# Kernel optimization log

Hardware: AMD Instinct MI355X
Metric: run time of the kernel (lower is better)

Reference implementation:

```python
import jax, jax.numpy as jnp
import numpy as np

KH = KW = 3
K = KH * KW
OG = 1  # offset_groups
WG = 1  # weight_groups
DIL = 1

def _conv_same(x, w):
    # stride-1 SAME NCHW conv, matching the keras offset/mask convs
    return jax.lax.conv_general_dilated(
        x, w, window_strides=(1, 1), padding='SAME',
        dimension_numbers=('NCHW', 'OIHW', 'NCHW'))

def _deform_conv2d(x, w, offset, mask):
    # x: [B,C,H,W]; w: [F, C//WG, KH, KW]
    # offset: [B, OG*2*K, H, W] laid out as (og, k, {dy,dx});
    # mask:   [B, OG*K, H, W]
    B, C, H, W = x.shape
    F = w.shape[0]
    pad_h = ((KH - 1) * DIL) // 2
    pad_w = ((KW - 1) * DIL) // 2
    ky = jnp.arange(KH) * DIL - pad_h
    kx = jnp.arange(KW) * DIL - pad_w
    kyy, kxx = jnp.meshgrid(ky, kx, indexing='ij')
    kyy = kyy.reshape(K).astype(x.dtype)
    kxx = kxx.reshape(K).astype(x.dtype)

    off = offset.reshape(B, OG, K, 2, H, W)
    dy = off[:, :, :, 0]  # [B,OG,K,H,W]
    dx = off[:, :, :, 1]
    oy = jnp.arange(H, dtype=x.dtype)
    ox = jnp.arange(W, dtype=x.dtype)
    y = oy[None, None, None, :, None] + kyy[None, None, :, None, None] + dy
    xq = ox[None, None, None, None, :] + kxx[None, None, :, None, None] + dx

    y0 = jnp.floor(y)
    x0 = jnp.floor(xq)
    wy = y - y0   # [B,OG,K,H,W]
    wx = xq - x0
    y0i = y0.astype(jnp.int32)
    x0i = x0.astype(jnp.int32)

    Cg = C // OG
    xg = x.reshape(B, OG, Cg, H * W)

    def gather(yi, xi):
        valid = (yi >= 0) & (yi < H) & (xi >= 0) & (xi < W)
        idx = jnp.clip(yi, 0, H - 1) * W + jnp.clip(xi, 0, W - 1)
        flat = idx.reshape(B, OG, 1, K * H * W)
        v = jnp.take_along_axis(xg, flat, axis=3)   # [B,OG,Cg,K*H*W]
        v = v.reshape(B, OG, Cg, K, H, W)
        return v * valid[:, :, None].astype(x.dtype)

    v00 = gather(y0i, x0i)
    v01 = gather(y0i, x0i + 1)
    v10 = gather(y0i + 1, x0i)
    v11 = gather(y0i + 1, x0i + 1)
    wy_ = wy[:, :, None]
    wx_ = wx[:, :, None]
    samp = (v00 * (1 - wy_) * (1 - wx_) + v01 * (1 - wy_) * wx_
            + v10 * wy_ * (1 - wx_) + v11 * wy_ * wx_)  # [B,OG,Cg,K,H,W]
    m = mask.reshape(B, OG, K, H, W)[:, :, None]
    samp = samp * m
    wr = w.reshape(F, OG, Cg, K)
    return jnp.einsum('bgckhw,fgck->bfhw', samp, wr)


def setup_inputs() -> dict:
    key = jax.random.key(0)
    k1, k2, k3, k4 = jax.random.split(key, 4)
    B, C, H, W = 8, 256, 64, 64
    F = 256
    x = jax.random.normal(k1, (B, C, H, W), dtype=jnp.float32)
    w_offset = jax.random.normal(k2, (OG * 2 * K, C, KH, KW), dtype=jnp.float32) * 0.01
    w_mask = jax.random.normal(k3, (OG * K, C, KH, KW), dtype=jnp.float32) * 0.01
    w_deform = jax.random.normal(k4, (F, C // WG, KH, KW), dtype=jnp.float32) * 0.05
    return {'x': x, 'w_offset': w_offset, 'w_mask': w_mask, 'w_deform': w_deform}


def reference(x, w_offset, w_mask, w_deform):
    offset = _conv_same(x, w_offset)                 # [B, 2K, H, W]
    mask = jax.nn.sigmoid(_conv_same(x, w_mask))     # [B, K, H, W]
    return _deform_conv2d(x, w_deform, offset, mask)
```

## Files before the change

### kernel.cpp

```cpp
#include <hip/hip_runtime.h>
#include <hip/hip_bf16.h>
#include <hip/hip_fp16.h>
#include <math.h>

constexpr int Bn = 8, Cn = 256, Hn = 64, Wn = 64, Fn = 256, Kn = 9;
constexpr int HWn = Hn * Wn;
constexpr int NM = Bn * Kn * HWn;
constexpr int NCH = 4;

using frag_ab = __attribute__((ext_vector_type(8))) short;
using frag_h  = __attribute__((ext_vector_type(8))) _Float16;
using f32x4   = __attribute__((ext_vector_type(4))) float;

__device__ inline ushort f2bf(float f) {
    union { float f; uint32_t u; } un{f};
    return (ushort)((un.u + 0x7FFF + ((un.u >> 16) & 1)) >> 16);
}
__device__ inline ushort f2h(float f) {
    __half h = __float2half_rn(f);
    return *reinterpret_cast<ushort*>(&h);
}

__global__ __launch_bounds__(256) void wpack27(const float* __restrict__ wo,
                                               const float* __restrict__ wm,
                                               ushort* __restrict__ wA) {
    int i = blockIdx.x * 256 + threadIdx.x;
    if (i >= 73728) return;
    int ci = i & 7, l = (i >> 3) & 63, mt = (i >> 9) & 1, cblk = (i >> 10) & 7, tap = i >> 13;
    int m = mt * 16 + (l & 15);
    int c = cblk * 32 + ((l >> 4) & 3) * 8 + ci;
    float v = 0.f;
    if (m < 18)      v = wo[(m * Cn + c) * 9 + tap];
    else if (m < 27) v = wm[((m - 18) * Cn + c) * 9 + tap];
    wA[i] = f2bf(v);
}

__global__ __launch_bounds__(256) void offconv27(const float* __restrict__ x,
                                                 const ushort* __restrict__ wA,
                                                 float* __restrict__ part) {
    __shared__ ushort xs[4][66][40];
    const int t = threadIdx.x;
    const int l = t & 63, w = t >> 6;
    const int li = l & 15, lg = l >> 4;
    const int rb = blockIdx.x, ch = blockIdx.y, b = blockIdx.z;
    const int h0 = rb * 2;
    const int rw = w >> 1, pt0 = (w & 1) * 2;

    f32x4 acc[2][2];
#pragma unroll
    for (int mt = 0; mt < 2; ++mt)
#pragma unroll
        for (int q = 0; q < 2; ++q) acc[mt][q] = (f32x4)0.f;

    const float* xb = x + (size_t)b * Cn * HWn;

#pragma unroll 1
    for (int cc = 0; cc < 2; ++cc) {
        const int cbase = ch * 64 + cc * 32;
        __syncthreads();
        for (int j = t; j < 1056; j += 256) {
            int cq = j / 264;
            int rem = j - cq * 264;
            int r = rem / 66, col = rem - r * 66;
            int rg = h0 - 1 + r, cg = col - 1;
            ushort u[8];
            if ((unsigned)rg < (unsigned)Hn && (unsigned)cg < (unsigned)Wn) {
                const float* xp = xb + (size_t)(cbase + cq * 8) * HWn + (rg << 6) + cg;
#pragma unroll
                for (int jj = 0; jj < 8; ++jj) u[jj] = f2bf(xp[(size_t)jj * HWn]);
            } else {
#pragma unroll
                for (int jj = 0; jj < 8; ++jj) u[jj] = 0;
            }
            *(int4*)&xs[r][col][cq * 8] =
                make_int4(u[0] | (u[1] << 16), u[2] | (u[3] << 16),
                          u[4] | (u[5] << 16), u[6] | (u[7] << 16));
        }
        __syncthreads();
        const int cblk = ch * 2 + cc;
#pragma unroll
        for (int tap = 0; tap < 9; ++tap) {
            const int ky = tap / 3, kx = tap - 3 * (tap / 3);
            frag_ab a0 = *(const frag_ab*)(wA + (size_t)((tap * 8 + cblk) * 2) * 512 + l * 8);
            frag_ab a1 = *(const frag_ab*)(wA + (size_t)((tap * 8 + cblk) * 2 + 1) * 512 + l * 8);
#pragma unroll
            for (int q = 0; q < 2; ++q) {
                frag_ab bf = *(const frag_ab*)&xs[rw + ky][(pt0 + q) * 16 + li + kx][lg * 8];
                acc[0][q] = __builtin_amdgcn_mfma_f32_16x16x32_bf16(a0, bf, acc[0][q], 0, 0, 0);
                acc[1][q] = __builtin_amdgcn_mfma_f32_16x16x32_bf16(a1, bf, acc[1][q], 0, 0, 0);
            }
        }
    }

    const int h = h0 + rw;
#pragma unroll
    for (int mt = 0; mt < 2; ++mt)
#pragma unroll
        for (int j = 0; j < 4; ++j) {
            int m = mt * 16 + lg * 4 + j;
            if (m < 27) {
#pragma unroll
                for (int q = 0; q < 2; ++q) {
                    int pixel = (pt0 + q) * 16 + li;
                    part[((size_t)((ch * Bn + b) * 27 + m) << 12) + (h << 6) + pixel] =
                        acc[mt][q][j];
                }
            }
        }
}

__global__ __launch_bounds__(256) void metafin9(const float* __restrict__ part,
                                                int4* __restrict__ mpack) {
    const int k = blockIdx.y;
    const int idx = blockIdx.x * 256 + threadIdx.x;
    const int b = idx >> 12, p = idx & 4095;
    const int h = p >> 6, w = p & 63;

    float dy = 0.f, dx = 0.f, ms = 0.f;
#pragma unroll
    for (int ch = 0; ch < NCH; ++ch) {
        size_t base = ((size_t)((ch * Bn + b) * 27) << 12) + p;
        dy += part[base + ((size_t)(2 * k) << 12)];
        dx += part[base + ((size_t)(2 * k + 1) << 12)];
        ms += part[base + ((size_t)(18 + k) << 12)];
    }
    float m = 1.f / (1.f + expf(-ms));
    float yy = (float)(h + k / 3 - 1) + dy;
    float xx = (float)(w + k % 3 - 1) + dx;
    float y0f = floorf(yy), x0f = floorf(xx);
    float wy = yy - y0f, wx = xx - x0f;
    int y0 = (int)y0f, x0 = (int)x0f;
    int y1 = y0 + 1, x1 = x0 + 1;
    bool vy0 = (unsigned)y0 < (unsigned)Hn;
    bool vx0 = (unsigned)x0 < (unsigned)Wn;
    bool vy1 = (unsigned)y1 < (unsigned)Hn;
    bool vx1 = (unsigned)x1 < (unsigned)Wn;
    int cy0 = min(max(y0, 0), Hn - 1), cx0 = min(max(x0, 0), Wn - 1);
    int cy1 = min(max(y1, 0), Hn - 1), cx1 = min(max(x1, 0), Wn - 1);
    float w00 = (vy0 && vx0) ? (1.f - wy) * (1.f - wx) * m : 0.f;
    float w01 = (vy0 && vx1) ? (1.f - wy) * wx * m : 0.f;
    float w10 = (vy1 && vx0) ? wy * (1.f - wx) * m : 0.f;
    float w11 = (vy1 && vx1) ? wy * wx * m : 0.f;
    int i00 = (cy0 << 6) + cx0, i01 = (cy0 << 6) + cx1;
    int i10 = (cy1 << 6) + cx0, i11 = (cy1 << 6) + cx1;
    union { struct { __half a, bh; } h; int i; } pz, pw;
    pz.h.a = __float2half_rn(w00); pz.h.bh = __float2half_rn(w01);
    pw.h.a = __float2half_rn(w10); pw.h.bh = __float2half_rn(w11);
    int q = ((b * 9 + k) << 12) + p;
    mpack[q] = make_int4(i00 | (i01 << 16), i10 | (i11 << 16), pz.i, pw.i);
}

__global__ __launch_bounds__(256) void packBX(const float* __restrict__ wd,
                                              const float* __restrict__ x,
                                              ushort* __restrict__ wB,
                                              __half2* __restrict__ xh) {
    const int bid = blockIdx.x, t = threadIdx.x;
    if (bid < 2304) {
        int i = bid * 256 + t;
        int ci = i & 7, fi = (i >> 3) & 15, G = (i >> 7) & 31, ft = (i >> 12) & 15, k = i >> 16;
        int f = ft * 16 + fi, c = G * 8 + ci;
        wB[i] = f2h(wd[(f * Cn + c) * 9 + k]);
    } else {
        int i = (bid - 2304) * 256 + t;
        int p = i & 4095, q = (i >> 12) & 3, b = i >> 14;
        const float* xp = x + (size_t)b * Cn * HWn + p;
        __half2* op = xh + (((size_t)b * 4096 + p) << 7) + q * 32;
#pragma unroll
        for (int j = 0; j < 32; ++j) {
            int c = q * 64 + 2 * j;
            op[j] = __float22half2_rn(make_float2(xp[(size_t)c * HWn],
                                                  xp[(size_t)(c + 1) * HWn]));
        }
    }
}

__global__ __launch_bounds__(512, 4) void dconv(const uint32_t* __restrict__ xh,
                                                const ushort* __restrict__ wB,
                                                const int4* __restrict__ mpack,
                                                float* __restrict__ out) {
    __shared__ ushort sl[2][2][64][64];
    __shared__ int4 ml[9][64];
    const int t = threadIdx.x;
    const int l = t & 63, w = t >> 6;
    const int li = l & 15, lg = l >> 4;
    const int pu = (w << 3) + (l >> 3);
    const int g  = l & 7;
    const int b = blockIdx.x;
    const int p0 = blockIdx.y << 6;

    f32x4 acc[2][4];
#pragma unroll
    for (int a = 0; a < 2; ++a)
#pragma unroll
        for (int q = 0; q < 4; ++q) acc[a][q] = (f32x4)0.f;

    const uint32_t* xb = xh + ((size_t)b << 19);

    for (int j = t; j < 576; j += 512)
        ml[j >> 6][j & 63] = mpack[((b * 9 + (j >> 6)) << 12) + p0 + (j & 63)];
    __syncthreads();

    auto STAGE = [&](int s) {
        const int k = s % 9, ch = s / 9;
        const int4 m = ml[k][pu];
        const int i00 = m.x & 0xFFFF, i01 = ((unsigned)m.x) >> 16;
        const int i10 = m.y & 0xFFFF, i11 = ((unsigned)m.y) >> 16;
        union { int i; __half2 h; } uz, uw;
        uz.i = m.z; uw.i = m.w;
        const uint32_t* base = xb + (ch << 5) + (g << 2);
        uint4 v00 = *(const uint4*)(base + (size_t)i00 * 128);
        uint4 v01 = *(const uint4*)(base + (size_t)i01 * 128);
        uint4 v10 = *(const uint4*)(base + (size_t)i10 * 128);
        uint4 v11 = *(const uint4*)(base + (size_t)i11 * 128);
        const __half2 w00 = __half2half2(__low2half(uz.h));
        const __half2 w01 = __half2half2(__high2half(uz.h));
        const __half2 w10 = __half2half2(__low2half(uw.h));
        const __half2 w11 = __half2half2(__high2half(uw.h));
        uint4 rr;
        {
            __half2 r = __hmul2(w00, *(__half2*)&v00.x);
            r = __hfma2(w01, *(__half2*)&v01.x, r);
            r = __hfma2(w10, *(__half2*)&v10.x, r);
            r = __hfma2(w11, *(__half2*)&v11.x, r);
            rr.x = *(uint32_t*)&r;
        }
        {
            __half2 r = __hmul2(w00, *(__half2*)&v00.y);
            r = __hfma2(w01, *(__half2*)&v01.y, r);
            r = __hfma2(w10, *(__half2*)&v10.y, r);
            r = __hfma2(w11, *(__half2*)&v11.y, r);
            rr.y = *(uint32_t*)&r;
        }
        {
            __half2 r = __hmul2(w00, *(__half2*)&v00.z);
            r = __hfma2(w01, *(__half2*)&v01.z, r);
            r = __hfma2(w10, *(__half2*)&v10.z, r);
            r = __hfma2(w11, *(__half2*)&v11.z, r);
            rr.z = *(uint32_t*)&r;
        }
        {
            __half2 r = __hmul2(w00, *(__half2*)&v00.w);
            r = __hfma2(w01, *(__half2*)&v01.w, r);
            r = __hfma2(w10, *(__half2*)&v10.w, r);
            r = __hfma2(w11, *(__half2*)&v11.w, r);
            rr.w = *(uint32_t*)&r;
        }
        *(uint4*)&sl[(s >> 1) & 1][s & 1][pu][(g ^ (pu & 7)) << 3] = rr;
    };

    auto COMPUTE = [&](int s) {
        const int k = s % 9, ch = s / 9;
        const ushort* wp = wB + ((size_t)((k * 16 + 2 * w) * 512 + ch * 128)) * 8;
#pragma unroll
        for (int h = 0; h < 2; ++h) {
            frag_h bq[4];
#pragma unroll
            for (int pt = 0; pt < 4; ++pt)
                bq[pt] = *(const frag_h*)&sl[(s >> 1) & 1][s & 1][pt * 16 + li]
                                           [((((h << 2) | lg) ^ (l & 7)) << 3)];
#pragma unroll
            for (int ft = 0; ft < 2; ++ft) {
                frag_h a = *(const frag_h*)(wp + (size_t)(ft * 512 + h * 64 + l) * 8);
#pragma unroll
                for (int pt = 0; pt < 4; ++pt)
                    acc[ft][pt] = __builtin_amdgcn_mfma_f32_16x16x32_f16(
                        a, bq[pt], acc[ft][pt], 0, 0, 0);
            }
        }
    };

    STAGE(0);
    STAGE(1);
    __syncthreads();
#pragma unroll 1
    for (int s = 0; s < 36; s += 2) {
        if (s + 2 < 36) {
            STAGE(s + 2);
            STAGE(s + 3);
        }
        COMPUTE(s);
        COMPUTE(s + 1);
        __syncthreads();
    }

    float* ob = out + (size_t)b * Fn * HWn + p0;
#pragma unroll
    for (int ft = 0; ft < 2; ++ft)
#pragma unroll
        for (int j = 0; j < 4; ++j) {
            int f = w * 32 + ft * 16 + lg * 4 + j;
#pragma unroll
            for (int pt = 0; pt < 4; ++pt)
                ob[(size_t)f * HWn + pt * 16 + li] = acc[ft][pt][j];
        }
}

extern "C" void kernel_launch(void* const* d_in, const int* in_sizes, int n_in,
                              void* d_out, int out_size, void* d_ws, size_t ws_size,
                              hipStream_t stream) {
    const float* x  = (const float*)d_in[0];
    const float* wo = (const float*)d_in[1];
    const float* wm = (const float*)d_in[2];
    const float* wd = (const float*)d_in[3];
    float* out = (float*)d_out;

    int4*     mpack = (int4*)d_ws;
    char*     region = (char*)d_ws + (size_t)NM * 16;
    float*    part  = (float*)region;
    ushort*   wBp   = (ushort*)region;
    __half2*  xhh   = (__half2*)(region + 1179648);
    uint32_t* xhu   = (uint32_t*)(region + 1179648);
    ushort*   wA27  = (ushort*)(region + 18874368);

    wpack27<<<dim3(288), dim3(256), 0, stream>>>(wo, wm, wA27);
    offconv27<<<dim3(32, NCH, Bn), dim3(256), 0, stream>>>(x, wA27, part);
    metafin9<<<dim3(Bn * HWn / 256, 9), dim3(256), 0, stream>>>(part, mpack);
    packBX<<<dim3(2816), dim3(256), 0, stream>>>(wd, x, wBp, xhh);
    dconv<<<dim3(Bn, HWn / 64), dim3(512), 0, stream>>>(xhu, wBp, mpack, out);
}
```

Measured before the change: 105.7 us.

## Fuse offset conv with metadata finalisation and reuse packed fp16 input

Measured after the change: 110.2 us. +4.3%, slower.

```diff
diff --git a/kernel.cpp b/kernel.cpp
--- a/kernel.cpp
+++ b/kernel.cpp
@@ -6,162 +6,39 @@
 constexpr int Bn = 8, Cn = 256, Hn = 64, Wn = 64, Fn = 256, Kn = 9;
 constexpr int HWn = Hn * Wn;
 constexpr int NM = Bn * Kn * HWn;
-constexpr int NCH = 4;
-
-using frag_ab = __attribute__((ext_vector_type(8))) short;
+
 using frag_h  = __attribute__((ext_vector_type(8))) _Float16;
 using f32x4   = __attribute__((ext_vector_type(4))) float;
 
-__device__ inline ushort f2bf(float f) {
-    union { float f; uint32_t u; } un{f};
-    return (ushort)((un.u + 0x7FFF + ((un.u >> 16) & 1)) >> 16);
-}
 __device__ inline ushort f2h(float f) {
     __half h = __float2half_rn(f);
     return *reinterpret_cast<ushort*>(&h);
 }
 
-__global__ __launch_bounds__(256) void wpack27(const float* __restrict__ wo,
+__global__ __launch_bounds__(256) void packall(const float* __restrict__ wd,
+                                               const float* __restrict__ wo,
                                                const float* __restrict__ wm,
-                                               ushort* __restrict__ wA) {
-    int i = blockIdx.x * 256 + threadIdx.x;
-    if (i >= 73728) return;
-    int ci = i & 7, l = (i >> 3) & 63, mt = (i >> 9) & 1, cblk = (i >> 10) & 7, tap = i >> 13;
-    int m = mt * 16 + (l & 15);
-    int c = cblk * 32 + ((l >> 4) & 3) * 8 + ci;
-    float v = 0.f;
-    if (m < 18)      v = wo[(m * Cn + c) * 9 + tap];
-    else if (m < 27) v = wm[((m - 18) * Cn + c) * 9 + tap];
-    wA[i] = f2bf(v);
-}
-
-__global__ __launch_bounds__(256) void offconv27(const float* __restrict__ x,
-                                                 const ushort* __restrict__ wA,
-                                                 float* __restrict__ part) {
-    __shared__ ushort xs[4][66][40];
-    const int t = threadIdx.x;
-    const int l = t & 63, w = t >> 6;
-    const int li = l & 15, lg = l >> 4;
-    const int rb = blockIdx.x, ch = blockIdx.y, b = blockIdx.z;
-    const int h0 = rb * 2;
-    const int rw = w >> 1, pt0 = (w & 1) * 2;
-
-    f32x4 acc[2][2];
-#pragma unroll
-    for (int mt = 0; mt < 2; ++mt)
-#pragma unroll
-        for (int q = 0; q < 2; ++q) acc[mt][q] = (f32x4)0.f;
-
-    const float* xb = x + (size_t)b * Cn * HWn;
-
-#pragma unroll 1
-    for (int cc = 0; cc < 2; ++cc) {
-        const int cbase = ch * 64 + cc * 32;
-        __syncthreads();
-        for (int j = t; j < 1056; j += 256) {
-            int cq = j / 264;
-            int rem = j - cq * 264;
-            int r = rem / 66, col = rem - r * 66;
-            int rg = h0 - 1 + r, cg = col - 1;
-            ushort u[8];
-            if ((unsigned)rg < (unsigned)Hn && (unsigned)cg < (unsigned)Wn) {
-                const float* xp = xb + (size_t)(cbase + cq * 8) * HWn + (rg << 6) + cg;
-#pragma unroll
-                for (int jj = 0; jj < 8; ++jj) u[jj] = f2bf(xp[(size_t)jj * HWn]);
-            } else {
-#pragma unroll
-                for (int jj = 0; jj < 8; ++jj) u[jj] = 0;
-            }
-            *(int4*)&xs[r][col][cq * 8] =
-                make_int4(u[0] | (u[1] << 16), u[2] | (u[3] << 16),
-                          u[4] | (u[5] << 16), u[6] | (u[7] << 16));
-        }
-        __syncthreads();
-        const int cblk = ch * 2 + cc;
-#pragma unroll
-        for (int tap = 0; tap < 9; ++tap) {
-            const int ky = tap / 3, kx = tap - 3 * (tap / 3);
-            frag_ab a0 = *(const frag_ab*)(wA + (size_t)((tap * 8 + cblk) * 2) * 512 + l * 8);
-            frag_ab a1 = *(const frag_ab*)(wA + (size_t)((tap * 8 + cblk) * 2 + 1) * 512 + l * 8);
-#pragma unroll
-            for (int q = 0; q < 2; ++q) {
-                frag_ab bf = *(const frag_ab*)&xs[rw + ky][(pt0 + q) * 16 + li + kx][lg * 8];
-                acc[0][q] = __builtin_amdgcn_mfma_f32_16x16x32_bf16(a0, bf, acc[0][q], 0, 0, 0);
-                acc[1][q] = __builtin_amdgcn_mfma_f32_16x16x32_bf16(a1, bf, acc[1][q], 0, 0, 0);
-            }
-        }
-    }
-
-    const int h = h0 + rw;
-#pragma unroll
-    for (int mt = 0; mt < 2; ++mt)
-#pragma unroll
-        for (int j = 0; j < 4; ++j) {
-            int m = mt * 16 + lg * 4 + j;
-            if (m < 27) {
-#pragma unroll
-                for (int q = 0; q < 2; ++q) {
-                    int pixel = (pt0 + q) * 16 + li;
-                    part[((size_t)((ch * Bn + b) * 27 + m) << 12) + (h << 6) + pixel] =
-                        acc[mt][q][j];
-                }
-            }
-        }
-}
-
-__global__ __launch_bounds__(256) void metafin9(const float* __restrict__ part,
-                                                int4* __restrict__ mpack) {
-    const int k = blockIdx.y;
-    const int idx = blockIdx.x * 256 + threadIdx.x;
-    const int b = idx >> 12, p = idx & 4095;
-    const int h = p >> 6, w = p & 63;
-
-    float dy = 0.f, dx = 0.f, ms = 0.f;
-#pragma unroll
-    for (int ch = 0; ch < NCH; ++ch) {
-        size_t base = ((size_t)((ch * Bn + b) * 27) << 12) + p;
-        dy += part[base + ((size_t)(2 * k) << 12)];
-        dx += part[base + ((size_t)(2 * k + 1) << 12)];
-        ms += part[base + ((size_t)(18 + k) << 12)];
-    }
-    float m = 1.f / (1.f + expf(-ms));
-    float yy = (float)(h + k / 3 - 1) + dy;
-    float xx = (float)(w + k % 3 - 1) + dx;
-    float y0f = floorf(yy), x0f = floorf(xx);
-    float wy = yy - y0f, wx = xx - x0f;
-    int y0 = (int)y0f, x0 = (int)x0f;
-    int y1 = y0 + 1, x1 = x0 + 1;
-    bool vy0 = (unsigned)y0 < (unsigned)Hn;
-    bool vx0 = (unsigned)x0 < (unsigned)Wn;
-    bool vy1 = (unsigned)y1 < (unsigned)Hn;
-    bool vx1 = (unsigned)x1 < (unsigned)Wn;
-    int cy0 = min(max(y0, 0), Hn - 1), cx0 = min(max(x0, 0), Wn - 1);
-    int cy1 = min(max(y1, 0), Hn - 1), cx1 = min(max(x1, 0), Wn - 1);
-    float w00 = (vy0 && vx0) ? (1.f - wy) * (1.f - wx) * m : 0.f;
-    float w01 = (vy0 && vx1) ? (1.f - wy) * wx * m : 0.f;
-    float w10 = (vy1 && vx0) ? wy * (1.f - wx) * m : 0.f;
-    float w11 = (vy1 && vx1) ? wy * wx * m : 0.f;
-    int i00 = (cy0 << 6) + cx0, i01 = (cy0 << 6) + cx1;
-    int i10 = (cy1 << 6) + cx0, i11 = (cy1 << 6) + cx1;
-    union { struct { __half a, bh; } h; int i; } pz, pw;
-    pz.h.a = __float2half_rn(w00); pz.h.bh = __float2half_rn(w01);
-    pw.h.a = __float2half_rn(w10); pw.h.bh = __float2half_rn(w11);
-    int q = ((b * 9 + k) << 12) + p;
-    mpack[q] = make_int4(i00 | (i01 << 16), i10 | (i11 << 16), pz.i, pw.i);
-}
-
-__global__ __launch_bounds__(256) void packBX(const float* __restrict__ wd,
-                                              const float* __restrict__ x,
-                                              ushort* __restrict__ wB,
-                                              __half2* __restrict__ xh) {
+                                               const float* __restrict__ x,
+                                               ushort* __restrict__ wB,
+                                               ushort* __restrict__ wA,
+                                               __half2* __restrict__ xh) {
     const int bid = blockIdx.x, t = threadIdx.x;
     if (bid < 2304) {
         int i = bid * 256 + t;
         int ci = i & 7, fi = (i >> 3) & 15, G = (i >> 7) & 31, ft = (i >> 12) & 15, k = i >> 16;
         int f = ft * 16 + fi, c = G * 8 + ci;
         wB[i] = f2h(wd[(f * Cn + c) * 9 + k]);
+    } else if (bid < 2592) {
+        int i = (bid - 2304) * 256 + t;
+        int ci = i & 7, l = (i >> 3) & 63, mt = (i >> 9) & 1, cblk = (i >> 10) & 7, tap = i >> 13;
+        int m = mt * 16 + (l & 15);
+        int c = cblk * 32 + ((l >> 4) & 3) * 8 + ci;
+        float v = 0.f;
+        if (m < 18)      v = wo[(m * Cn + c) * 9 + tap];
+        else if (m < 27) v = wm[((m - 18) * Cn + c) * 9 + tap];
+        wA[i] = f2h(v);
     } else {
-        int i = (bid - 2304) * 256 + t;
+        int i = (bid - 2592) * 256 + t;
         int p = i & 4095, q = (i >> 12) & 3, b = i >> 14;
         const float* xp = x + (size_t)b * Cn * HWn + p;
         __half2* op = xh + (((size_t)b * 4096 + p) << 7) + q * 32;
@@ -171,6 +48,99 @@
             op[j] = __float22half2_rn(make_float2(xp[(size_t)c * HWn],
                                                   xp[(size_t)(c + 1) * HWn]));
         }
+    }
+}
+
+__global__ __launch_bounds__(256) void offmeta(const uint32_t* __restrict__ xh,
+                                               const ushort* __restrict__ wA,
+                                               int4* __restrict__ mpack) {
+    __shared__ ushort xs[4][66][36];
+    __shared__ float macc[32][128];
+    const int t = threadIdx.x;
+    const int l = t & 63, w = t >> 6;
+    const int li = l & 15, lg = l >> 4;
+    const int rb = blockIdx.x, b = blockIdx.y;
+    const int h0 = rb * 2;
+    const int rw = w >> 1, pt0 = (w & 1) * 2;
+
+    f32x4 acc[2][2];
+#pragma unroll
+    for (int mt = 0; mt < 2; ++mt)
+#pragma unroll
+        for (int q = 0; q < 2; ++q) acc[mt][q] = (f32x4)0.f;
+
+    const uint32_t* xbb = xh + ((size_t)b << 19);
+
+#pragma unroll 1
+    for (int cs = 0; cs < 8; ++cs) {
+        __syncthreads();
+        for (int j = t; j < 1056; j += 256) {
+            int pj = j >> 2, qd = j & 3;
+            int r = pj / 66, col = pj - r * 66;
+            int rg = h0 - 1 + r, cg = col - 1;
+            uint4 v = make_uint4(0, 0, 0, 0);
+            if ((unsigned)rg < (unsigned)Hn && (unsigned)cg < (unsigned)Wn)
+                v = *(const uint4*)(xbb + ((size_t)((rg << 6) + cg) << 7) + cs * 16 + qd * 4);
+            *(uint4*)&xs[r][col][qd * 8] = v;
+        }
+        __syncthreads();
+#pragma unroll
+        for (int tap = 0; tap < 9; ++tap) {
+            const int ky = tap / 3, kx = tap - 3 * (tap / 3);
+            frag_h a0 = *(const frag_h*)(wA + (size_t)((tap * 8 + cs) * 2) * 512 + l * 8);
+            frag_h a1 = *(const frag_h*)(wA + (size_t)((tap * 8 + cs) * 2 + 1) * 512 + l * 8);
+#pragma unroll
+            for (int q = 0; q < 2; ++q) {
+                frag_h bf = *(const frag_h*)&xs[rw + ky][(pt0 + q) * 16 + li + kx][lg * 8];
+                acc[0][q] = __builtin_amdgcn_mfma_f32_16x16x32_f16(a0, bf, acc[0][q], 0, 0, 0);
+                acc[1][q] = __builtin_amdgcn_mfma_f32_16x16x32_f16(a1, bf, acc[1][q], 0, 0, 0);
+            }
+        }
+    }
+
+    __syncthreads();
+#pragma unroll
+    for (int mt = 0; mt < 2; ++mt)
+#pragma unroll
+        for (int j = 0; j < 4; ++j) {
+            int m = mt * 16 + lg * 4 + j;
+#pragma unroll
+            for (int q = 0; q < 2; ++q)
+                macc[m][rw * 64 + (pt0 + q) * 16 + li] = acc[mt][q][j];
+        }
+    __syncthreads();
+
+    for (int it = t; it < 1152; it += 256) {
+        int k = it >> 7, pxl = it & 127;
+        float dy = macc[2 * k][pxl];
+        float dx = macc[2 * k + 1][pxl];
+        float ms = macc[18 + k][pxl];
+        int h = h0 + (pxl >> 6), wc = pxl & 63;
+        float m = 1.f / (1.f + expf(-ms));
+        float yy = (float)(h + k / 3 - 1) + dy;
+        float xx = (float)(wc + k % 3 - 1) + dx;
+        float y0f = floorf(yy), x0f = floorf(xx);
+        float wy = yy - y0f, wx = xx - x0f;
+        int y0 = (int)y0f, x0 = (int)x0f;
+        int y1 = y0 + 1, x1 = x0 + 1;
+        bool vy0 = (unsigned)y0 < (unsigned)Hn;
+        bool vx0 = (unsigned)x0 < (unsigned)Wn;
+        bool vy1 = (unsigned)y1 < (unsigned)Hn;
+        bool vx1 = (unsigned)x1 < (unsigned)Wn;
+        int cy0 = min(max(y0, 0), Hn - 1), cx0 = min(max(x0, 0), Wn - 1);
+        int cy1 = min(max(y1, 0), Hn - 1), cx1 = min(max(x1, 0), Wn - 1);
+        float w00 = (vy0 && vx0) ? (1.f - wy) * (1.f - wx) * m : 0.f;
+        float w01 = (vy0 && vx1) ? (1.f - wy) * wx * m : 0.f;
+        float w10 = (vy1 && vx0) ? wy * (1.f - wx) * m : 0.f;
+        float w11 = (vy1 && vx1) ? wy * wx * m : 0.f;
+        int i00 = (cy0 << 6) + cx0, i01 = (cy0 << 6) + cx1;
+        int i10 = (cy1 << 6) + cx0, i11 = (cy1 << 6) + cx1;
+        union { struct { __half a, bh; } hh; int i; } pz, pw;
+        pz.hh.a = __float2half_rn(w00); pz.hh.bh = __float2half_rn(w01);
+        pw.hh.a = __float2half_rn(w10); pw.hh.bh = __float2half_rn(w11);
+        int p = (h << 6) + wc;
+        mpack[((b * 9 + k) << 12) + p] =
+            make_int4(i00 | (i01 << 16), i10 | (i11 << 16), pz.i, pw.i);
     }
 }
 
@@ -305,16 +275,12 @@
     float* out = (float*)d_out;
 
     int4*     mpack = (int4*)d_ws;
-    char*     region = (char*)d_ws + (size_t)NM * 16;
-    float*    part  = (float*)region;
-    ushort*   wBp   = (ushort*)region;
-    __half2*  xhh   = (__half2*)(region + 1179648);
-    uint32_t* xhu   = (uint32_t*)(region + 1179648);
-    ushort*   wA27  = (ushort*)(region + 18874368);
-
-    wpack27<<<dim3(288), dim3(256), 0, stream>>>(wo, wm, wA27);
-    offconv27<<<dim3(32, NCH, Bn), dim3(256), 0, stream>>>(x, wA27, part);
-    metafin9<<<dim3(Bn * HWn / 256, 9), dim3(256), 0, stream>>>(part, mpack);
-    packBX<<<dim3(2816), dim3(256), 0, stream>>>(wd, x, wBp, xhh);
+    ushort*   wBp   = (ushort*)((char*)d_ws + 4718592);
+    __half2*  xhh   = (__half2*)((char*)d_ws + 5898240);
+    uint32_t* xhu   = (uint32_t*)((char*)d_ws + 5898240);
+    ushort*   wA27  = (ushort*)((char*)d_ws + 22675456);
+
+    packall<<<dim3(3104), dim3(256), 0, stream>>>(wd, wo, wm, x, wBp, wA27, xhh);
+    offmeta<<<dim3(32, Bn), dim3(256), 0, stream>>>(xhu, wA27, mpack);
     dconv<<<dim3(Bn, HWn / 64), dim3(512), 0, stream>>>(xhu, wBp, mpack, out);
 }
```
